# Kernel tuning notes

Measured on AMD Instinct MI355X. Metric: run time of the kernel, lower is better.

Reference implementation:

```python
import jax, jax.numpy as jnp
import numpy as np

NEG_SLOPE = 0.01  # torch nn.LeakyReLU default


def setup_inputs() -> dict:
    key = jax.random.key(0)
    k1, k2, k3 = jax.random.split(key, 3)
    B, N, D = 16, 1024, 256
    i_em = jax.random.normal(k1, (B, N, D), dtype=jnp.float32)
    # att_a: Linear(2D -> 1); weight flattened to [2D], scalar bias [1]
    a_w = jax.random.normal(k2, (2 * D,), dtype=jnp.float32) * (1.0 / np.sqrt(2 * D))
    a_b = jax.random.normal(k3, (1,), dtype=jnp.float32) * 0.01
    return {"i_em": i_em, "a_w": a_w, "a_b": a_b}


def reference(i_em, a_w, a_b):
    # Original: cat(query_i, key_j) @ a_w + b over all (i, j) pairs, which
    # splits algebraically: score[b,i,j] = i_em[b,i] @ a_w[:D] + i_em[b,j] @ a_w[D:] + b
    D = i_em.shape[-1]
    aq, ak = a_w[:D], a_w[D:]
    q = jnp.einsum('bnd,d->bn', i_em, aq)  # [B, N]
    k = jnp.einsum('bnd,d->bn', i_em, ak)  # [B, N]
    scores = q[:, :, None] + k[:, None, :] + a_b[0]  # [B, N, N]
    scores = jnp.where(scores >= 0, scores, NEG_SLOPE * scores)  # LeakyReLU
    # dropout is identity in eval mode
    alphas = jax.nn.softmax(scores, axis=-1)  # over key dim j
    return alphas[..., None]  # [B, N, N, 1]
```

## Files before the change

### kernel.cpp

```cpp
#include <hip/hip_runtime.h>
#include <hip/hip_bf16.h>

#define NEG_SLOPE 0.01f

#define B_DIM 16
#define N_DIM 1024
#define D_DIM 256
#define ROWS (B_DIM * N_DIM)

typedef float fvec4 __attribute__((ext_vector_type(4)));

__device__ __forceinline__ float wave_reduce_sum(float v) {
#pragma unroll
    for (int off = 32; off > 0; off >>= 1) v += __shfl_xor(v, off, 64);
    return v;
}

__global__ __launch_bounds__(256) void qk_kernel(const float* __restrict__ i_em,
                                                 const float* __restrict__ a_w,
                                                 const float* __restrict__ a_b,
                                                 float* __restrict__ qb,
                                                 float* __restrict__ k) {
    const int wid  = threadIdx.x >> 6;
    const int lane = threadIdx.x & 63;
    const int row0 = blockIdx.x * 16 + wid * 4;

    const float4 wq = *reinterpret_cast<const float4*>(a_w + lane * 4);
    const float4 wk = *reinterpret_cast<const float4*>(a_w + D_DIM + lane * 4);
    const float bias = a_b[0];

    float4 e[4];
#pragma unroll
    for (int r = 0; r < 4; ++r)
        e[r] = *reinterpret_cast<const float4*>(i_em + (size_t)(row0 + r) * D_DIM + lane * 4);

    float sq[4], sk[4];
#pragma unroll
    for (int r = 0; r < 4; ++r) {
        sq[r] = e[r].x * wq.x + e[r].y * wq.y + e[r].z * wq.z + e[r].w * wq.w;
        sk[r] = e[r].x * wk.x + e[r].y * wk.y + e[r].z * wk.z + e[r].w * wk.w;
    }
#pragma unroll
    for (int r = 0; r < 4; ++r) {
        sq[r] = wave_reduce_sum(sq[r]);
        sk[r] = wave_reduce_sum(sk[r]);
    }

    if (lane == 0) {
        fvec4 vq = {sq[0] + bias, sq[1] + bias, sq[2] + bias, sq[3] + bias};
        fvec4 vk = {sk[0], sk[1], sk[2], sk[3]};
        *reinterpret_cast<fvec4*>(qb + row0) = vq;
        *reinterpret_cast<fvec4*>(k + row0)  = vk;
    }
}

__global__ __launch_bounds__(256) void softmax_kernel(const float* __restrict__ qb,
                                                      const float* __restrict__ k,
                                                      float* __restrict__ out) {
    const int wid  = threadIdx.x >> 6;
    const int lane = threadIdx.x & 63;
    const int row0 = blockIdx.x * 16 + wid * 4;
    const int b    = row0 >> 10;

    const float4* k4 = reinterpret_cast<const float4*>(k + b * N_DIM);
    float4 kv[4];
#pragma unroll
    for (int c = 0; c < 4; ++c) kv[c] = k4[c * 64 + lane];

    const fvec4 qv = *reinterpret_cast<const fvec4*>(qb + row0);

#pragma unroll
    for (int r = 0; r < 4; ++r) {
        const float qi = qv[r];

        float e[4][4];
        float s = 0.0f;
#pragma unroll
        for (int c = 0; c < 4; ++c) {
            float v0 = qi + kv[c].x; v0 = (v0 >= 0.0f) ? v0 : NEG_SLOPE * v0;
            float v1 = qi + kv[c].y; v1 = (v1 >= 0.0f) ? v1 : NEG_SLOPE * v1;
            float v2 = qi + kv[c].z; v2 = (v2 >= 0.0f) ? v2 : NEG_SLOPE * v2;
            float v3 = qi + kv[c].w; v3 = (v3 >= 0.0f) ? v3 : NEG_SLOPE * v3;
            e[c][0] = __expf(v0);
            e[c][1] = __expf(v1);
            e[c][2] = __expf(v2);
            e[c][3] = __expf(v3);
            s += (e[c][0] + e[c][1]) + (e[c][2] + e[c][3]);
        }
        s = wave_reduce_sum(s);
        const float inv = __builtin_amdgcn_rcpf(s);

        float4* o4 = reinterpret_cast<float4*>(out + (size_t)(row0 + r) * N_DIM);
#pragma unroll
        for (int c = 0; c < 4; ++c) {
            float4 o;
            o.x = e[c][0] * inv;
            o.y = e[c][1] * inv;
            o.z = e[c][2] * inv;
            o.w = e[c][3] * inv;
            o4[c * 64 + lane] = o;
        }
    }
}

extern "C" void kernel_launch(void* const* d_in, const int* in_sizes, int n_in,
                              void* d_out, int out_size, void* d_ws, size_t ws_size,
                              hipStream_t stream) {
    const float* i_em = (const float*)d_in[0];
    const float* a_w  = (const float*)d_in[1];
    const float* a_b  = (const float*)d_in[2];
    float* out = (float*)d_out;

    float* qb = (float*)d_ws;
    float* k  = qb + ROWS;

    qk_kernel<<<ROWS / 16, 256, 0, stream>>>(i_em, a_w, a_b, qb, k);
    softmax_kernel<<<ROWS / 16, 256, 0, stream>>>(qb, k, out);
}
```

Before: 22.54 us.

## Fuse projection and softmax into one kernel with per-block k recompute

Merges the q/k projection kernel and the softmax kernel into one launch. Each block recomputes the full k vector for its batch into shared memory and computes q for its 64 rows. This removes the second launch and the workspace round trip. The cost is that every block redundantly reads the whole batch slice of the input, multiplying input traffic by 16, and the grid becomes 256 large blocks.

```diff
diff --git a/kernel.cpp b/kernel.cpp
--- a/kernel.cpp
+++ b/kernel.cpp
@@ -16,62 +16,69 @@
     return v;
 }
 
-__global__ __launch_bounds__(256) void qk_kernel(const float* __restrict__ i_em,
-                                                 const float* __restrict__ a_w,
-                                                 const float* __restrict__ a_b,
-                                                 float* __restrict__ qb,
-                                                 float* __restrict__ k) {
+__global__ __launch_bounds__(1024) void fused_kernel(const float* __restrict__ i_em,
+                                                     const float* __restrict__ a_w,
+                                                     const float* __restrict__ a_b,
+                                                     float* __restrict__ out) {
+    __shared__ float k_lds[N_DIM];
+    __shared__ float q_lds[64];
+
     const int wid  = threadIdx.x >> 6;
     const int lane = threadIdx.x & 63;
-    const int row0 = blockIdx.x * 16 + wid * 4;
+    const int bi   = blockIdx.x;
+    const int batch = bi >> 4;
+
+    const float* slice = i_em + (size_t)batch * N_DIM * D_DIM;
 
     const float4 wq = *reinterpret_cast<const float4*>(a_w + lane * 4);
     const float4 wk = *reinterpret_cast<const float4*>(a_w + D_DIM + lane * 4);
     const float bias = a_b[0];
 
-    float4 e[4];
+    for (int it = 0; it < 16; ++it) {
+        const int j = wid * 64 + it * 4;
+        float sk[4];
 #pragma unroll
-    for (int r = 0; r < 4; ++r)
-        e[r] = *reinterpret_cast<const float4*>(i_em + (size_t)(row0 + r) * D_DIM + lane * 4);
+        for (int r = 0; r < 4; ++r) {
+            const float4 e = *reinterpret_cast<const float4*>(
+                slice + (size_t)(j + r) * D_DIM + lane * 4);
+            sk[r] = e.x * wk.x + e.y * wk.y + e.z * wk.z + e.w * wk.w;
+        }
+#pragma unroll
+        for (int r = 0; r < 4; ++r) sk[r] = wave_reduce_sum(sk[r]);
+        if (lane == 0) {
+            fvec4 v = {sk[0], sk[1], sk[2], sk[3]};
+            *reinterpret_cast<fvec4*>(&k_lds[j]) = v;
+        }
+    }
 
-    float sq[4], sk[4];
+    {
+        const int jq = (bi & 15) * 64 + wid * 4;
+        float sq[4];
+#pragma unroll
+        for (int r = 0; r < 4; ++r) {
+            const float4 e = *reinterpret_cast<const float4*>(
+                slice + (size_t)(jq + r) * D_DIM + lane * 4);
+            sq[r] = e.x * wq.x + e.y * wq.y + e.z * wq.z + e.w * wq.w;
+        }
+#pragma unroll
+        for (int r = 0; r < 4; ++r) sq[r] = wave_reduce_sum(sq[r]);
+        if (lane == 0) {
+            fvec4 v = {sq[0] + bias, sq[1] + bias, sq[2] + bias, sq[3] + bias};
+            *reinterpret_cast<fvec4*>(&q_lds[wid * 4]) = v;
+        }
+    }
+
+    __syncthreads();
+
+    float4 kv[4];
+#pragma unroll
+    for (int c = 0; c < 4; ++c)
+        kv[c] = *reinterpret_cast<const float4*>(&k_lds[(c * 64 + lane) * 4]);
+
+    const size_t orow0 = (size_t)bi * 64 + wid * 4;
 #pragma unroll
     for (int r = 0; r < 4; ++r) {
-        sq[r] = e[r].x * wq.x + e[r].y * wq.y + e[r].z * wq.z + e[r].w * wq.w;
-        sk[r] = e[r].x * wk.x + e[r].y * wk.y + e[r].z * wk.z + e[r].w * wk.w;
-    }
-#pragma unroll
-    for (int r = 0; r < 4; ++r) {
-        sq[r] = wave_reduce_sum(sq[r]);
-        sk[r] = wave_reduce_sum(sk[r]);
-    }
-
-    if (lane == 0) {
-        fvec4 vq = {sq[0] + bias, sq[1] + bias, sq[2] + bias, sq[3] + bias};
-        fvec4 vk = {sk[0], sk[1], sk[2], sk[3]};
-        *reinterpret_cast<fvec4*>(qb + row0) = vq;
-        *reinterpret_cast<fvec4*>(k + row0)  = vk;
-    }
-}
-
-__global__ __launch_bounds__(256) void softmax_kernel(const float* __restrict__ qb,
-                                                      const float* __restrict__ k,
-                                                      float* __restrict__ out) {
-    const int wid  = threadIdx.x >> 6;
-    const int lane = threadIdx.x & 63;
-    const int row0 = blockIdx.x * 16 + wid * 4;
-    const int b    = row0 >> 10;
-
-    const float4* k4 = reinterpret_cast<const float4*>(k + b * N_DIM);
-    float4 kv[4];
-#pragma unroll
-    for (int c = 0; c < 4; ++c) kv[c] = k4[c * 64 + lane];
-
-    const fvec4 qv = *reinterpret_cast<const fvec4*>(qb + row0);
-
-#pragma unroll
-    for (int r = 0; r < 4; ++r) {
-        const float qi = qv[r];
+        const float qi = q_lds[wid * 4 + r];
 
         float e[4][4];
         float s = 0.0f;
@@ -90,7 +97,7 @@
         s = wave_reduce_sum(s);
         const float inv = __builtin_amdgcn_rcpf(s);
 
-        float4* o4 = reinterpret_cast<float4*>(out + (size_t)(row0 + r) * N_DIM);
+        float4* o4 = reinterpret_cast<float4*>(out + (orow0 + r) * N_DIM);
 #pragma unroll
         for (int c = 0; c < 4; ++c) {
             float4 o;
@@ -111,9 +118,5 @@
     const float* a_b  = (const float*)d_in[2];
     float* out = (float*)d_out;
 
-    float* qb = (float*)d_ws;
-    float* k  = qb + ROWS;
-
-    qk_kernel<<<ROWS / 16, 256, 0, stream>>>(i_em, a_w, a_b, qb, k);
-    softmax_kernel<<<ROWS / 16, 256, 0, stream>>>(qb, k, out);
+    fused_kernel<<<256, 1024, 0, stream>>>(i_em, a_w, a_b, out);
 }
```

New measurement: 39.32 us. 74.4% more time.
